# Kernel tuning notes

Hardware: AMD Instinct MI355X
Metric: run time of the kernel (lower is better)

## Reference

```python
import jax, jax.numpy as jnp
import numpy as np

HIDDEN = 1024
NUM_HEADS = 16
HEAD_DIM = HIDDEN // NUM_HEADS
ROPE_THETA = 10000.0


def rope_tables(seq_len, head_dim, theta):
    inv_freq = 1.0 / theta ** (jnp.arange(0, head_dim, 2, dtype=jnp.float32) / head_dim)
    pos = jnp.arange(seq_len, dtype=jnp.float32)
    freqs = jnp.outer(pos, inv_freq)  # [S, hd/2]
    return jnp.cos(freqs), jnp.sin(freqs)


def apply_rope(x, cos, sin):
    # x: [B, nh, S, hd]; cos/sin: [S, hd/2]
    x1, x2 = jnp.split(x, 2, axis=-1)
    return jnp.concatenate([x1 * cos - x2 * sin, x2 * cos + x1 * sin], axis=-1)


def setup_inputs() -> dict:
    key = jax.random.key(0)
    k1, k2, k3 = jax.random.split(key, 3)
    B, S = 2, 2048
    hidden_states = jax.random.normal(k1, (B, S, HIDDEN), dtype=jnp.float32)
    # nn.Linear stores weight as [out, in]; y = x @ W.T
    Wqkv = jax.random.normal(k2, (3 * HIDDEN, HIDDEN), dtype=jnp.float32) * (HIDDEN ** -0.5)
    Wo = jax.random.normal(k3, (HIDDEN, HIDDEN), dtype=jnp.float32) * (HIDDEN ** -0.5)
    return {"hidden_states": hidden_states, "Wqkv": Wqkv, "Wo": Wo}


def reference(hidden_states, Wqkv, Wo):
    B, S, H = hidden_states.shape
    qkv = hidden_states @ Wqkv.T  # [B, S, 3H]
    qkv = qkv.reshape(B, S, 3, NUM_HEADS, HEAD_DIM)
    q, k, v = jnp.moveaxis(qkv, 2, 0)  # each [B, S, nh, hd]
    q = jnp.transpose(q, (0, 2, 1, 3))  # [B, nh, S, hd]
    k = jnp.transpose(k, (0, 2, 1, 3))
    v = jnp.transpose(v, (0, 2, 1, 3))
    cos, sin = rope_tables(S, HEAD_DIM, ROPE_THETA)
    q = apply_rope(q, cos, sin)
    k = apply_rope(k, cos, sin)
    scale = 1.0 / jnp.sqrt(jnp.asarray(HEAD_DIM, dtype=q.dtype))
    scores = jnp.einsum("bhqd,bhkd->bhqk", q, k) * scale
    causal = jnp.tril(jnp.ones((S, S), dtype=bool))
    scores = jnp.where(causal, scores, jnp.finfo(scores.dtype).min)
    attn = jax.nn.softmax(scores, axis=-1)
    out = jnp.einsum("bhqk,bhkd->bhqd", attn, v)  # [B, nh, S, hd]
    out = jnp.transpose(out, (0, 2, 1, 3)).reshape(B, S, H)
    return out @ Wo.T
```

## Files before the change

### kernel.cpp

```cpp
#include <hip/hip_runtime.h>
#include <hip/hip_bf16.h>
#include <math.h>

typedef __bf16 bf16_t;
typedef __attribute__((ext_vector_type(8))) __bf16 bf16x8;
typedef __attribute__((ext_vector_type(4))) float f32x4;
typedef __attribute__((ext_vector_type(16))) float f32x16;
typedef __attribute__((ext_vector_type(4))) unsigned u32x4;

#define AS1(p) ((__attribute__((address_space(1))) void*)(p))
#define AS3(p) ((__attribute__((address_space(3))) void*)(p))

__device__ inline void cvt8(const float* __restrict__ in, bf16_t* __restrict__ out, int i) {
  const float4* p = (const float4*)in;
  float4 a = p[2 * i], b = p[2 * i + 1];
  bf16x8 o;
  o[0] = (bf16_t)a.x; o[1] = (bf16_t)a.y; o[2] = (bf16_t)a.z; o[3] = (bf16_t)a.w;
  o[4] = (bf16_t)b.x; o[5] = (bf16_t)b.y; o[6] = (bf16_t)b.z; o[7] = (bf16_t)b.w;
  ((bf16x8*)out)[i] = o;
}

__global__ __launch_bounds__(256)
void prep_all(const float* __restrict__ hid, const float* __restrict__ wqkv,
              const float* __restrict__ wo, bf16_t* __restrict__ hidb,
              bf16_t* __restrict__ wqkvb, bf16_t* __restrict__ wob,
              float* __restrict__ cosb, float* __restrict__ sinb) {
  const int bid = blockIdx.x, tid = threadIdx.x;
  if (bid < 2048) {
    cvt8(hid, hidb, bid * 256 + tid);
  } else if (bid < 3584) {
    cvt8(wqkv, wqkvb, (bid - 2048) * 256 + tid);
  } else if (bid < 4096) {
    cvt8(wo, wob, (bid - 3584) * 256 + tid);
  } else {
    int t = (bid - 4096) * 256 + tid;
    int s = t >> 5, i = t & 31;
    float inv = powf(10000.0f, -(float)i / 32.0f);
    float sv, cv;
    sincosf((float)s * inv, &sv, &cv);
    cosb[t] = cv;
    sinb[t] = sv;
  }
}

__global__ __launch_bounds__(256)
void pack_rope(bf16_t* __restrict__ qkv, const float* __restrict__ cosb,
               const float* __restrict__ sinb, bf16_t* __restrict__ Kp) {
  const int t = blockIdx.x, bh = blockIdx.y, b = bh >> 4, h = bh & 15;
  const int tid = threadIdx.x;
  const int r = tid >> 2, j = tid & 3;
  const int s = t * 64 + r;
  bf16_t* base = qkv + ((size_t)(b * 2048 + s)) * 3072 + h * 64;
  const float* cb = cosb + s * 32 + j * 8;
  const float* sb = sinb + s * 32 + j * 8;
  bf16x8 q1 = *(const bf16x8*)(base + j * 8);
  bf16x8 q2 = *(const bf16x8*)(base + j * 8 + 32);
  bf16x8 k1 = *(const bf16x8*)(base + 1024 + j * 8);
  bf16x8 k2 = *(const bf16x8*)(base + 1024 + j * 8 + 32);
  const float QS = 0.125f * 1.4426950408889634f;
  bf16x8 qo1, qo2, ko1, ko2;
#pragma unroll
  for (int i = 0; i < 8; ++i) {
    float c = cb[i], sn = sb[i];
    float a1 = (float)q1[i], a2 = (float)q2[i];
    qo1[i] = (bf16_t)((a1 * c - a2 * sn) * QS);
    qo2[i] = (bf16_t)((a2 * c + a1 * sn) * QS);
    float b1 = (float)k1[i], b2 = (float)k2[i];
    ko1[i] = (bf16_t)(b1 * c - b2 * sn);
    ko2[i] = (bf16_t)(b2 * c + b1 * sn);
  }
  *(bf16x8*)(base + j * 8) = qo1;
  *(bf16x8*)(base + j * 8 + 32) = qo2;
  bf16_t* kd = Kp + ((size_t)(bh * 32 + t)) * 4096 + r * 64;
  *(bf16x8*)(kd + ((j ^ (r & 7)) * 8)) = ko1;
  *(bf16x8*)(kd + (((j + 4) ^ (r & 7)) * 8)) = ko2;
}

__global__ __launch_bounds__(256)
void pack_v(bf16_t* __restrict__ qkv) {
  __shared__ bf16_t vl[64][72];
  const int t = blockIdx.x, bh = blockIdx.y, b = bh >> 4, hd = bh & 15;
  const int tid = threadIdx.x;
  const int r = tid >> 2, j = tid & 3;
  const bf16_t* vsrc = qkv + ((size_t)(b * 2048 + t * 64 + r)) * 3072 + 2048 + hd * 64;
  bf16x8 v1 = *(const bf16x8*)(vsrc + j * 8);
  bf16x8 v2 = *(const bf16x8*)(vsrc + j * 8 + 32);
#pragma unroll
  for (int i = 0; i < 8; ++i) { vl[r][j * 8 + i] = v1[i]; vl[r][j * 8 + 32 + i] = v2[i]; }
  __syncthreads();
  const int g = tid >> 5, l0 = tid & 31;
  const int d = (g < 4) ? l0 : (32 + l0);
  const int ch0 = 2 * (g & 3);
  bf16x8 f0, f1;
#pragma unroll
  for (int i = 0; i < 8; ++i) { f0[i] = vl[8 * ch0 + i][d]; f1[i] = vl[8 * ch0 + 8 + i][d]; }
  bf16_t* dst = qkv + ((size_t)(b * 2048 + t * 64 + hd * 4 + (g >> 1))) * 3072 + 1024 + (g & 1) * 512;
  *(bf16x8*)(dst + l0 * 8) = f0;
  *(bf16x8*)(dst + (l0 + 32) * 8) = f1;
}

template <typename OutT>
__global__ __launch_bounds__(256, 2)
void gemm_nt(const bf16_t* __restrict__ A, const bf16_t* __restrict__ B,
             OutT* __restrict__ C, int M, int N, int K) {
  __shared__ __align__(16) bf16_t lA[128 * 64];
  __shared__ __align__(16) bf16_t lB[128 * 64];
  const int tid = threadIdx.x;
  const int wid = tid >> 6, lane = tid & 63;
  const int lr = lane & 15, lg = lane >> 4;
  const int nwg = gridDim.x * gridDim.y;
  int lin = blockIdx.y * gridDim.x + blockIdx.x;
  lin = (lin & 7) * (nwg >> 3) + (lin >> 3);
  const int m0 = (lin / gridDim.x) * 128, n0 = (lin % gridDim.x) * 128;
  const int wm = (wid >> 1) * 64, wn = (wid & 1) * 64;
  const int srow = lane >> 3;
  const int scol = (lane & 7) * 8;
  f32x4 acc[4][4];
#pragma unroll
  for (int i = 0; i < 4; ++i)
#pragma unroll
    for (int j = 0; j < 4; ++j) acc[i][j] = f32x4{0.f, 0.f, 0.f, 0.f};

  const int nk = K >> 6;
  for (int kt = 0; kt < nk; ++kt) {
    const int k0 = kt << 6;
    __syncthreads();
#pragma unroll
    for (int i = 0; i < 4; ++i) {
      int c = (wid << 2) + i;
      int r = (c << 3) + srow;
      __builtin_amdgcn_global_load_lds(AS1(A + (size_t)(m0 + r) * K + k0 + scol),
                                       AS3(&lA[c * 512]), 16, 0, 0);
      __builtin_amdgcn_global_load_lds(AS1(B + (size_t)(n0 + r) * K + k0 + scol),
                                       AS3(&lB[c * 512]), 16, 0, 0);
    }
    __syncthreads();
#pragma unroll
    for (int ks = 0; ks < 2; ++ks) {
      bf16x8 af[4], bfr[4];
#pragma unroll
      for (int i = 0; i < 4; ++i) {
        af[i]  = *(const bf16x8*)&lA[(wm + i * 16 + lr) * 64 + ks * 32 + lg * 8];
        bfr[i] = *(const bf16x8*)&lB[(wn + i * 16 + lr) * 64 + ks * 32 + lg * 8];
      }
#pragma unroll
      for (int i = 0; i < 4; ++i)
#pragma unroll
        for (int j = 0; j < 4; ++j)
          acc[i][j] = __builtin_amdgcn_mfma_f32_16x16x32_bf16(af[i], bfr[j], acc[i][j], 0, 0, 0);
    }
  }
#pragma unroll
  for (int i = 0; i < 4; ++i)
#pragma unroll
    for (int j = 0; j < 4; ++j)
#pragma unroll
      for (int r = 0; r < 4; ++r) {
        int row = m0 + wm + i * 16 + lg * 4 + r;
        int col = n0 + wn + j * 16 + lr;
        C[(size_t)row * N + col] = (OutT)acc[i][j][r];
      }
}

__device__ inline unsigned pkbf(float a, float b) {
  bf16_t x = (bf16_t)a, y = (bf16_t)b;
  return (unsigned)__builtin_bit_cast(unsigned short, x) |
         ((unsigned)__builtin_bit_cast(unsigned short, y) << 16);
}
__device__ inline f32x16 zero16() {
  f32x16 z;
#pragma unroll
  for (int r = 0; r < 16; ++r) z[r] = 0.f;
  return z;
}

__device__ const unsigned char ROLE_LUT[44] = {
    19, 18, 17, 16,
    15, 95, 159, 158,
    14, 94, 93, 157,
    13, 92, 156, 91, 155, 154,
    12, 90, 89, 153, 152,
    11, 88, 87, 151, 150,
    10, 86, 85, 149, 148,
    9, 84,
    8, 7, 6, 5, 4, 3, 2, 1, 0};

__global__ __launch_bounds__(128, 4)
void attn_fwd(const bf16_t* __restrict__ qkv, const bf16_t* __restrict__ Kp,
              bf16_t* __restrict__ O, bf16_t* __restrict__ Po, float* __restrict__ Plp) {
  __shared__ __align__(16) bf16_t Ksh[2][4096];
  const int tid = threadIdx.x, wid = tid >> 6, lane = tid & 63;
  const int ln = lane & 31, h = lane >> 5;
  const int lin = blockIdx.x;
  const int e = ROLE_LUT[lin >> 5];
  const int bh = lin & 31;
  const int c = e & 31, kind = e >> 6;
  const int b = bh >> 4, hd = bh & 15;
  const int t0 = (kind == 2) ? ((c + 1) >> 1) : 0;
  const int t1 = (kind == 1) ? ((c + 1) >> 1) : c + 1;
  const int qw = c * 64 + wid * 32;

  const bf16_t* Qrow = qkv + ((size_t)(b * 2048 + qw + ln)) * 3072 + hd * 64;
  bf16x8 qf[4];
#pragma unroll
  for (int t = 0; t < 4; ++t) qf[t] = *(const bf16x8*)(Qrow + t * 16 + h * 8);

  f32x16 o0 = zero16(), o1 = zero16();
  float lpa = 0.f, lpb = 0.f, lpc = 0.f, lpd = 0.f;

  const bf16_t* Kbase = Kp + ((size_t)bh * 32) * 4096 + tid * 8;
  const bf16_t* Vp0 = qkv + ((size_t)(b * 2048 + hd * 4)) * 3072 + 1024 + lane * 8;

#define KSTAGE(T, BUF)                                                                    \
  do {                                                                                    \
    const bf16_t* ks = Kbase + (size_t)(T) * 4096;                                        \
    __builtin_amdgcn_global_load_lds(AS1(ks),        AS3(&Ksh[BUF][tid * 8]), 16, 0, 0);  \
    __builtin_amdgcn_global_load_lds(AS1(ks + 1024), AS3(&Ksh[BUF][1024 + tid * 8]), 16, 0, 0); \
    __builtin_amdgcn_global_load_lds(AS1(ks + 2048), AS3(&Ksh[BUF][2048 + tid * 8]), 16, 0, 0); \
    __builtin_amdgcn_global_load_lds(AS1(ks + 3072), AS3(&Ksh[BUF][3072 + tid * 8]), 16, 0, 0); \
  } while (0)

  KSTAGE(t0, t0 & 1);
  for (int t = t0; t < t1; ++t) {
    asm volatile("s_waitcnt vmcnt(0)" ::: "memory");
    __builtin_amdgcn_s_barrier();
    if (t + 1 < t1) KSTAGE(t + 1, (t + 1) & 1);
    const bf16_t* vb = Vp0 + (size_t)t * (64 * 3072);
    bf16x8 v0[4];
#pragma unroll
    for (int u = 0; u < 4; ++u)
      v0[u] = *(const bf16x8*)(vb + (u >> 1) * 3072 + (u & 1) * 512);
    const bf16_t* K = &Ksh[t & 1][0];
    f32x16 s0 = zero16(), s1 = zero16();
    __builtin_amdgcn_s_setprio(1);
#pragma unroll
    for (int u = 0; u < 4; ++u) {
      const int ch = 2 * u + h;
      bf16x8 k0 = *(const bf16x8*)&K[ln * 64 + ((ch ^ (ln & 7)) * 8)];
      bf16x8 k1 = *(const bf16x8*)&K[(32 + ln) * 64 + ((ch ^ (ln & 7)) * 8)];
      s0 = __builtin_amdgcn_mfma_f32_32x32x16_bf16(k0, qf[u], s0, 0, 0, 0);
      s1 = __builtin_amdgcn_mfma_f32_32x32x16_bf16(k1, qf[u], s1, 0, 0, 0);
    }
    __builtin_amdgcn_s_setprio(0);
    bf16x8 v1[4];
#pragma unroll
    for (int u = 0; u < 4; ++u)
      v1[u] = *(const bf16x8*)(vb + (2 + (u >> 1)) * 3072 + (u & 1) * 512);
    if (t == c) {
      const int qg = qw + ln, k0g = t * 64;
#pragma unroll
      for (int r = 0; r < 16; ++r) {
        int kv = k0g + (r & 3) + 8 * (r >> 2) + 4 * h;
        if (kv > qg) s0[r] = -3e38f;
        if (kv + 32 > qg) s1[r] = -3e38f;
      }
    }
#pragma unroll
    for (int r = 0; r < 16; r += 4) {
      float p0 = __builtin_amdgcn_exp2f(s0[r]);     lpa += p0; s0[r] = p0;
      float p1 = __builtin_amdgcn_exp2f(s0[r + 1]); lpb += p1; s0[r + 1] = p1;
      float p2 = __builtin_amdgcn_exp2f(s0[r + 2]); lpc += p2; s0[r + 2] = p2;
      float p3 = __builtin_amdgcn_exp2f(s0[r + 3]); lpd += p3; s0[r + 3] = p3;
      float p4 = __builtin_amdgcn_exp2f(s1[r]);     lpa += p4; s1[r] = p4;
      float p5 = __builtin_amdgcn_exp2f(s1[r + 1]); lpb += p5; s1[r + 1] = p5;
      float p6 = __builtin_amdgcn_exp2f(s1[r + 2]); lpc += p6; s1[r + 2] = p6;
      float p7 = __builtin_amdgcn_exp2f(s1[r + 3]); lpd += p7; s1[r + 3] = p7;
    }
    __builtin_amdgcn_s_setprio(1);
#pragma unroll
    for (int u = 0; u < 4; ++u) {
      const int w = u & 1;
      f32x16 sv = (u >> 1) ? s1 : s0;
      unsigned x  = pkbf(sv[8 * w + 0], sv[8 * w + 1]);
      unsigned x2 = pkbf(sv[8 * w + 2], sv[8 * w + 3]);
      unsigned y  = pkbf(sv[8 * w + 4], sv[8 * w + 5]);
      unsigned y2 = pkbf(sv[8 * w + 6], sv[8 * w + 7]);
      asm volatile("v_permlane32_swap_b32 %0, %1" : "+v"(x), "+v"(y));
      asm volatile("v_permlane32_swap_b32 %0, %1" : "+v"(x2), "+v"(y2));
      u32x4 pw; pw[0] = x; pw[1] = x2; pw[2] = y; pw[3] = y2;
      bf16x8 pf = __builtin_bit_cast(bf16x8, pw);
      o0 = __builtin_amdgcn_mfma_f32_32x32x16_bf16(v0[u], pf, o0, 0, 0, 0);
      o1 = __builtin_amdgcn_mfma_f32_32x32x16_bf16(v1[u], pf, o1, 0, 0, 0);
    }
    __builtin_amdgcn_s_setprio(0);
  }
#undef KSTAGE
  float lp = (lpa + lpb) + (lpc + lpd);
  float lpf = lp + __shfl_xor(lp, 32, 64);
  if (kind == 0) {
    float inv = 1.0f / lpf;
    bf16_t* Oaddr = O + ((size_t)(b * 2048 + qw + ln)) * 1024 + hd * 64;
#pragma unroll
    for (int D = 0; D < 2; ++D) {
      f32x16 ov = D ? o1 : o0;
#pragma unroll
      for (int Q = 0; Q < 4; ++Q) {
        uint2 w;
        w.x = pkbf(ov[4 * Q + 0] * inv, ov[4 * Q + 1] * inv);
        w.y = pkbf(ov[4 * Q + 2] * inv, ov[4 * Q + 3] * inv);
        *(uint2*)(Oaddr + D * 32 + Q * 8 + 4 * h) = w;
      }
    }
  } else {
    const int slot = (bh * 12 + (c - 20)) * 2 + (kind - 1);
    const int qi = wid * 32 + ln;
    if (h == 0) Plp[slot * 64 + qi] = lpf;
    bf16_t* Paddr = Po + ((size_t)(slot * 64 + qi)) * 64;
#pragma unroll
    for (int D = 0; D < 2; ++D) {
      f32x16 ov = D ? o1 : o0;
#pragma unroll
      for (int Q = 0; Q < 4; ++Q) {
        uint2 w;
        w.x = pkbf(ov[4 * Q + 0], ov[4 * Q + 1]);
        w.y = pkbf(ov[4 * Q + 2], ov[4 * Q + 3]);
        *(uint2*)(Paddr + D * 32 + Q * 8 + 4 * h) = w;
      }
    }
  }
}

__global__ __launch_bounds__(64)
void attn_combine(const bf16_t* __restrict__ Po, const float* __restrict__ Plp,
                  bf16_t* __restrict__ O) {
  const int blk = blockIdx.x;
  const int bh = blk / 12, sc = blk % 12;
  const int b = bh >> 4, hd = bh & 15;
  const int c = 20 + sc;
  const int q = threadIdx.x;
  const int slotA = (bh * 12 + sc) * 2, slotB = slotA + 1;
  float inv = 1.0f / (Plp[slotA * 64 + q] + Plp[slotB * 64 + q]);
  const bf16x8* pa = (const bf16x8*)(Po + ((size_t)(slotA * 64 + q)) * 64);
  const bf16x8* pb = (const bf16x8*)(Po + ((size_t)(slotB * 64 + q)) * 64);
  bf16_t* oaddr = O + ((size_t)(b * 2048 + c * 64 + q)) * 1024 + hd * 64;
#pragma unroll
  for (int j = 0; j < 8; ++j) {
    bf16x8 a = pa[j], v = pb[j];
    bf16x8 w;
#pragma unroll
    for (int k = 0; k < 8; ++k) w[k] = (bf16_t)(((float)a[k] + (float)v[k]) * inv);
    ((bf16x8*)oaddr)[j] = w;
  }
}

extern "C" void kernel_launch(void* const* d_in, const int* in_sizes, int n_in,
                              void* d_out, int out_size, void* d_ws, size_t ws_size,
                              hipStream_t stream) {
  const float* hid  = (const float*)d_in[0];
  const float* wqkv = (const float*)d_in[1];
  const float* wo   = (const float*)d_in[2];
  float* out = (float*)d_out;
  char* ws = (char*)d_ws;
  bf16_t* hidb  = (bf16_t*)(ws);
  bf16_t* wqkvb = (bf16_t*)(ws + 8388608);
  bf16_t* wob   = (bf16_t*)(ws + 14680064);
  bf16_t* qkvb  = (bf16_t*)(ws + 16777216);
  float*  cosb  = (float*)(ws + 41943040);
  float*  sinb  = (float*)(ws + 42205184);
  bf16_t* Ob    = (bf16_t*)(ws + 42467328);
  bf16_t* Kp    = (bf16_t*)(ws);
  bf16_t* Po    = (bf16_t*)(ws + 8388608);
  float*  Plp   = (float*)(ws + 41943040);

  prep_all<<<4352, 256, 0, stream>>>(hid, wqkv, wo, hidb, wqkvb, wob, cosb, sinb);
  gemm_nt<bf16_t><<<dim3(24, 32), 256, 0, stream>>>(hidb, wqkvb, qkvb, 4096, 3072, 1024);
  pack_rope<<<dim3(32, 32), 256, 0, stream>>>(qkvb, cosb, sinb, Kp);
  pack_v<<<dim3(32, 32), 256, 0, stream>>>(qkvb);
  attn_fwd<<<1408, 128, 0, stream>>>(qkvb, Kp, Ob, Po, Plp);
  attn_combine<<<384, 64, 0, stream>>>(Po, Plp, Ob);
  gemm_nt<float><<<dim3(8, 32), 256, 0, stream>>>(Ob, wob, out, 4096, 1024, 1024);
}
```

Baseline: 120.3 us.

## Split causal attention into fixed 8-tile KV chunks for all long query blocks

Replaces the old role table, which split only the last query blocks into two halves, with a uniform split-KV scheme. Every query block past the eighth is now divided into chunks of at most 8 KV tiles, giving 2560 equally sized work items. The combine kernel merges 2 to 4 partial results per query block. The aim is better load balance and occupancy across the CUs, at the cost of more partial-output traffic to new workspace regions and a larger combine pass.

```diff
diff --git a/kernel.cpp b/kernel.cpp
--- a/kernel.cpp
+++ b/kernel.cpp
@@ -174,16 +174,19 @@
   return z;
 }
 
-__device__ const unsigned char ROLE_LUT[44] = {
-    19, 18, 17, 16,
-    15, 95, 159, 158,
-    14, 94, 93, 157,
-    13, 92, 156, 91, 155, 154,
-    12, 90, 89, 153, 152,
-    11, 88, 87, 151, 150,
-    10, 86, 85, 149, 148,
-    9, 84,
-    8, 7, 6, 5, 4, 3, 2, 1, 0};
+__device__ const unsigned short ROLE16[80] = {
+    224, 256, 288, 320, 352, 384, 416, 448,
+    480, 488, 512, 520, 544, 552, 576, 584, 608, 616, 640, 648, 672, 680, 704, 712,
+    736, 744, 752, 768, 776, 784, 800, 808, 816, 832, 840, 848,
+    864, 872, 880, 896, 904, 912, 928, 936, 944, 960, 968, 976,
+    992, 1000, 1008, 1016,
+    192, 456, 720, 984,
+    160, 424, 688, 952,
+    128, 392, 656, 920,
+    96, 360, 624, 888,
+    64, 328, 592, 856,
+    32, 296, 560, 824,
+    0, 264, 528, 792};
 
 __global__ __launch_bounds__(128, 4)
 void attn_fwd(const bf16_t* __restrict__ qkv, const bf16_t* __restrict__ Kp,
@@ -192,12 +195,11 @@
   const int tid = threadIdx.x, wid = tid >> 6, lane = tid & 63;
   const int ln = lane & 31, h = lane >> 5;
   const int lin = blockIdx.x;
-  const int e = ROLE_LUT[lin >> 5];
+  const int role = ROLE16[lin >> 5];
   const int bh = lin & 31;
-  const int c = e & 31, kind = e >> 6;
+  const int c = role >> 5, t0 = role & 31;
+  const int t1 = min(t0 + 8, c + 1);
   const int b = bh >> 4, hd = bh & 15;
-  const int t0 = (kind == 2) ? ((c + 1) >> 1) : 0;
-  const int t1 = (kind == 1) ? ((c + 1) >> 1) : c + 1;
   const int qw = c * 64 + wid * 32;
 
   const bf16_t* Qrow = qkv + ((size_t)(b * 2048 + qw + ln)) * 3072 + hd * 64;
@@ -287,7 +289,7 @@
 #undef KSTAGE
   float lp = (lpa + lpb) + (lpc + lpd);
   float lpf = lp + __shfl_xor(lp, 32, 64);
-  if (kind == 0) {
+  if (c < 8) {
     float inv = 1.0f / lpf;
     bf16_t* Oaddr = O + ((size_t)(b * 2048 + qw + ln)) * 1024 + hd * 64;
 #pragma unroll
@@ -302,7 +304,11 @@
       }
     }
   } else {
-    const int slot = (bh * 12 + (c - 20)) * 2 + (kind - 1);
+    const int p = t0 >> 3;
+    const int local = (c < 16) ? (c - 8) * 2 + p
+                               : (c < 24) ? 16 + (c - 16) * 3 + p
+                                          : 40 + (c - 24) * 4 + p;
+    const int slot = bh * 72 + local;
     const int qi = wid * 32 + ln;
     if (h == 0) Plp[slot * 64 + qi] = lpf;
     bf16_t* Paddr = Po + ((size_t)(slot * 64 + qi)) * 64;
@@ -324,21 +330,31 @@
 void attn_combine(const bf16_t* __restrict__ Po, const float* __restrict__ Plp,
                   bf16_t* __restrict__ O) {
   const int blk = blockIdx.x;
-  const int bh = blk / 12, sc = blk % 12;
+  const int bh = blk / 24, cidx = blk % 24;
+  const int c = 8 + cidx;
   const int b = bh >> 4, hd = bh & 15;
-  const int c = 20 + sc;
   const int q = threadIdx.x;
-  const int slotA = (bh * 12 + sc) * 2, slotB = slotA + 1;
-  float inv = 1.0f / (Plp[slotA * 64 + q] + Plp[slotB * 64 + q]);
-  const bf16x8* pa = (const bf16x8*)(Po + ((size_t)(slotA * 64 + q)) * 64);
-  const bf16x8* pb = (const bf16x8*)(Po + ((size_t)(slotB * 64 + q)) * 64);
+  const int np = (c < 16) ? 2 : (c < 24) ? 3 : 4;
+  const int base = bh * 72 + ((c < 16) ? (c - 8) * 2
+                                       : (c < 24) ? 16 + (c - 16) * 3
+                                                  : 40 + (c - 24) * 4);
+  float lsum = 0.f;
+  for (int p = 0; p < np; ++p) lsum += Plp[(base + p) * 64 + q];
+  float inv = 1.0f / lsum;
   bf16_t* oaddr = O + ((size_t)(b * 2048 + c * 64 + q)) * 1024 + hd * 64;
 #pragma unroll
   for (int j = 0; j < 8; ++j) {
-    bf16x8 a = pa[j], v = pb[j];
+    float acc[8];
+#pragma unroll
+    for (int k = 0; k < 8; ++k) acc[k] = 0.f;
+    for (int p = 0; p < np; ++p) {
+      bf16x8 a = ((const bf16x8*)(Po + ((size_t)((base + p) * 64 + q)) * 64))[j];
+#pragma unroll
+      for (int k = 0; k < 8; ++k) acc[k] += (float)a[k];
+    }
     bf16x8 w;
 #pragma unroll
-    for (int k = 0; k < 8; ++k) w[k] = (bf16_t)(((float)a[k] + (float)v[k]) * inv);
+    for (int k = 0; k < 8; ++k) w[k] = (bf16_t)(acc[k] * inv);
     ((bf16x8*)oaddr)[j] = w;
   }
 }
@@ -359,14 +375,14 @@
   float*  sinb  = (float*)(ws + 42205184);
   bf16_t* Ob    = (bf16_t*)(ws + 42467328);
   bf16_t* Kp    = (bf16_t*)(ws);
-  bf16_t* Po    = (bf16_t*)(ws + 8388608);
-  float*  Plp   = (float*)(ws + 41943040);
+  bf16_t* Po    = (bf16_t*)(ws + 52428800);
+  float*  Plp   = (float*)(ws + 71303168);
 
   prep_all<<<4352, 256, 0, stream>>>(hid, wqkv, wo, hidb, wqkvb, wob, cosb, sinb);
   gemm_nt<bf16_t><<<dim3(24, 32), 256, 0, stream>>>(hidb, wqkvb, qkvb, 4096, 3072, 1024);
   pack_rope<<<dim3(32, 32), 256, 0, stream>>>(qkvb, cosb, sinb, Kp);
   pack_v<<<dim3(32, 32), 256, 0, stream>>>(qkvb);
-  attn_fwd<<<1408, 128, 0, stream>>>(qkvb, Kp, Ob, Po, Plp);
-  attn_combine<<<384, 64, 0, stream>>>(Po, Plp, Ob);
+  attn_fwd<<<2560, 128, 0, stream>>>(qkvb, Kp, Ob, Po, Plp);
+  attn_combine<<<768, 64, 0, stream>>>(Po, Plp, Ob);
   gemm_nt<float><<<dim3(8, 32), 256, 0, stream>>>(Ob, wob, out, 4096, 1024, 1024);
 }
```

Result: slower. 129.0 us (+7.2%).
